# Optimization experiments

Hardware: AMD Instinct MI355X
Metric: run time of the kernel (lower is better)

## Reference

```python
import jax, jax.numpy as jnp
import numpy as np

DIM = 128

def _complex_linear_params(key, dim, scale=0.05):
    k1, k2, k3, k4 = jax.random.split(key, 4)
    Wr = jax.random.normal(k1, (dim, dim), jnp.float32) * scale
    Wi = jax.random.normal(k2, (dim, dim), jnp.float32) * scale
    br = jax.random.normal(k3, (dim,), jnp.float32) * scale
    bi = jax.random.normal(k4, (dim,), jnp.float32) * scale
    return Wr, Wi, br, bi

def setup_inputs() -> dict:
    key = jax.random.key(0)
    ks = jax.random.split(key, 8)
    B, C, Ht, Wt = 8, DIM, 64, 64
    Hs, Ws = 32, 32
    inp = {
        'target_r': jax.random.normal(ks[0], (B, C, Ht, Wt), jnp.float32),
        'target_i': jax.random.normal(ks[1], (B, C, Ht, Wt), jnp.float32),
        'source_r': jax.random.normal(ks[2], (B, C, Hs, Ws), jnp.float32),
        'source_i': jax.random.normal(ks[3], (B, C, Hs, Ws), jnp.float32),
    }
    for name, k in zip(('q', 'k', 'v'), ks[4:7]):
        Wr, Wi, br, bi = _complex_linear_params(k, DIM)
        inp[f'W{name}_r'], inp[f'W{name}_i'] = Wr, Wi
        inp[f'b{name}_r'], inp[f'b{name}_i'] = br, bi
    inp['gamma'] = jnp.float32(0.1)
    return inp

def reference(target_r, target_i, source_r, source_i,
              Wq_r, Wq_i, bq_r, bq_i,
              Wk_r, Wk_i, bk_r, bk_i,
              Wv_r, Wv_i, bv_r, bv_i, gamma):
    B, C, Ht, Wt = target_r.shape
    _, _, Hs, Ws = source_r.shape
    Nt, Ns = Ht * Wt, Hs * Ws
    scale = jnp.float32(C ** 0.5)
    # complex tensors [B, N, C]
    t = (target_r + 1j * target_i).reshape(B, C, Nt).transpose(0, 2, 1)
    s = (source_r + 1j * source_i).reshape(B, C, Ns).transpose(0, 2, 1)
    Wq = Wq_r + 1j * Wq_i; Wk = Wk_r + 1j * Wk_i; Wv = Wv_r + 1j * Wv_i
    Q = jnp.einsum('bnc,dc->bnd', t, Wq) + (bq_r + 1j * bq_i)
    K = jnp.einsum('bmc,dc->bmd', s, Wk) + (bk_r + 1j * bk_i)
    V = jnp.einsum('bmc,dc->bmd', s, Wv) + (bv_r + 1j * bv_i)
    # complex QK^H, keep only real part for softmax
    attn = jnp.einsum('bnd,bmd->bnm', Q, jnp.conj(K))  # [B, Nt, Ns] complex
    w = jax.nn.softmax(attn.real / scale, axis=-1)      # real weights
    out = jnp.einsum('bnm,bmd->bnd', w.astype(V.dtype), V)  # complex [B, Nt, C]
    out = out.transpose(0, 2, 1).reshape(B, C, Ht, Wt)
    return gamma * out
```

## Files before the change

### kernel.cpp

```cpp
#include <hip/hip_runtime.h>
#include <hip/hip_bf16.h>

#define NB 8
#define NC 128
#define NT 4096
#define NS 1024

typedef short bf16x8 __attribute__((ext_vector_type(8)));
typedef float f32x4  __attribute__((ext_vector_type(4)));

#define MFMA16(a, b, c) __builtin_amdgcn_mfma_f32_16x16x32_bf16(a, b, c, 0, 0, 0)

__device__ __forceinline__ short f2b(float x) {
    __hip_bfloat16 h = __float2bfloat16(x);
    return *reinterpret_cast<short*>(&h);
}

__device__ __forceinline__ void gl_lds16(const void* g, void* l) {
    __builtin_amdgcn_global_load_lds(
        (const __attribute__((address_space(1))) unsigned int*)g,
        (__attribute__((address_space(3))) unsigned int*)l, 16, 0, 0);
}

__global__ __launch_bounds__(256) void pack_w_kernel(
    const float* __restrict__ Wqr, const float* __restrict__ Wqi,
    const float* __restrict__ Wkr, const float* __restrict__ Wki,
    const float* __restrict__ Wvr, const float* __restrict__ Wvi,
    __hip_bfloat16* __restrict__ WqT, __hip_bfloat16* __restrict__ WkT,
    __hip_bfloat16* __restrict__ WvT)
{
    const int idx = blockIdx.x * 256 + threadIdx.x;
    const float *Wr, *Wi; __hip_bfloat16* dst; int base;
    if (idx < 65536)       { Wr = Wqr; Wi = Wqi; dst = WqT; base = idx; }
    else if (idx < 131072) { Wr = Wkr; Wi = Wki; dst = WkT; base = idx - 65536; }
    else                   { Wr = Wvr; Wi = Wvi; dst = WvT; base = idx - 131072; }
    const int dp = base >> 8, k = base & 255;
    const int d  = dp & 127;
    float v;
    if (dp < 128) v = (k < 128) ? Wr[d * 128 + k] : -Wi[d * 128 + k - 128];
    else          v = (k < 128) ? Wi[d * 128 + k] :  Wr[d * 128 + k - 128];
    dst[base] = __float2bfloat16(v);
}

__global__ __launch_bounds__(256) void projKV_kernel(
    const float* __restrict__ Xr, const float* __restrict__ Xi,
    const __hip_bfloat16* __restrict__ WkT, const __hip_bfloat16* __restrict__ WvT,
    const float* __restrict__ bkr, const float* __restrict__ bki,
    const float* __restrict__ bvr,
    __hip_bfloat16* __restrict__ Kh, __hip_bfloat16* __restrict__ VrT)
{
    __shared__ __align__(16) char smem[27136];
    const int b   = blockIdx.x & 7;
    const int n0  = (blockIdx.x >> 3) * 32;
    const int tid = threadIdx.x;

    for (int i = tid; i < 32 * 64; i += 256) {
        const int cp = i >> 5, n = i & 31, c = cp * 2;
        const size_t rb = (size_t)(b * NC + c) * NS + n0 + n;
        const unsigned pr = (unsigned short)f2b(Xr[rb]) |
                            ((unsigned)(unsigned short)f2b(Xr[rb + NS]) << 16);
        const unsigned pi = (unsigned short)f2b(Xi[rb]) |
                            ((unsigned)(unsigned short)f2b(Xi[rb + NS]) << 16);
        *(unsigned*)(smem + n * 528 + c * 2)         = pr;
        *(unsigned*)(smem + n * 528 + (128 + c) * 2) = pi;
    }
    __syncthreads();

    const int w = tid >> 6, l15 = tid & 15, q = (tid & 63) >> 4;
    const int r0 = (w & 1) * 16;
    const int g  = w >> 1;

    const char* wp[12];
    #pragma unroll
    for (int jj = 0; jj < 12; ++jj) {
        const int j = g * 12 + jj;
        wp[jj] = (j < 16)
            ? (const char*)WkT + (size_t)(j * 16 + l15) * 512 + q * 16
            : (const char*)WvT + (size_t)((j - 16) * 16 + l15) * 512 + q * 16;
    }

    f32x4 acc[12];
    #pragma unroll
    for (int jj = 0; jj < 12; ++jj) { acc[jj][0]=0.f; acc[jj][1]=0.f; acc[jj][2]=0.f; acc[jj][3]=0.f; }

    #pragma unroll
    for (int t = 0; t < 8; ++t) {
        const bf16x8 af = *(const bf16x8*)(smem + (r0 + l15) * 528 + (t * 32 + q * 8) * 2);
        #pragma unroll
        for (int jj = 0; jj < 12; ++jj) {
            const bf16x8 bf = *(const bf16x8*)(wp[jj] + t * 64);
            acc[jj] = MFMA16(af, bf, acc[jj]);
        }
    }

    #pragma unroll
    for (int jj = 0; jj < 12; ++jj) {
        const int j = g * 12 + jj;
        if (j < 16) {
            const int col = j * 16 + l15;
            const float bv = (col < 128) ? bkr[col] : bki[col - 128];
            #pragma unroll
            for (int r = 0; r < 4; ++r) {
                const int n = n0 + r0 + q * 4 + r;
                Kh[((size_t)(b * NS + n) << 8) + col] = __float2bfloat16(acc[jj][r] + bv);
            }
        } else {
            const int d = (j - 16) * 16 + l15;
            #pragma unroll
            for (int r = 0; r < 4; ++r)
                *(__hip_bfloat16*)(smem + 16896 + d * 80 + (r0 + q * 4 + r) * 2) =
                    __float2bfloat16(acc[jj][r] + bvr[d]);
        }
    }
    __syncthreads();
    for (int i = tid; i < 128 * 4; i += 256) {
        const int d = i >> 2, seg = i & 3;
        const int4 v = *(const int4*)(smem + 16896 + d * 80 + seg * 16);
        *(int4*)((char*)VrT + ((size_t)(b * NC + d) * NS + n0) * 2 + seg * 16) = v;
    }
}

__device__ __forceinline__ void stage_chunk(const char* Kbase, const char* Vbase,
                                            char* buf, int ch, int w, int lane)
{
    const char* ks = Kbase + (size_t)ch * 16384;
    #pragma unroll
    for (int i = 0; i < 4; ++i) {
        const int ml = w * 8 + i * 2 + (lane >> 5);
        const int so = ml * 512 + (((lane & 31) ^ (ml & 7)) << 4);
        gl_lds16(ks + so, buf + (w * 4 + i) * 1024);
    }
    const char* vsrc = Vbase + (size_t)ch * 64;
    #pragma unroll
    for (int i = 0; i < 2; ++i) {
        const int d  = (w + i * 4) * 16 + (lane >> 2);
        const int so = d * 2048 + (((lane & 3) ^ ((lane >> 2) & 3)) << 4);
        gl_lds16(vsrc + so, buf + 16384 + (w + i * 4) * 1024);
    }
}

__global__ __launch_bounds__(256, 2) void attn_mfma_kernel(
    const float* __restrict__ tr_g, const float* __restrict__ ti_g,
    const __hip_bfloat16* __restrict__ WqT,
    const float* __restrict__ bqr, const float* __restrict__ bqi,
    const __hip_bfloat16* __restrict__ Kh, const __hip_bfloat16* __restrict__ VrT,
    const float* __restrict__ gamma_p, float* __restrict__ out)
{
    __shared__ __align__(16) char smem[78848];
    char* As = smem;
    char* ps = smem + 73728;

    const int b    = blockIdx.x & 7;
    const int n0   = (blockIdx.x >> 3) * 64;
    const int tid  = threadIdx.x;
    const int w    = tid >> 6, lane = tid & 63, l15 = tid & 15, q = (tid & 63) >> 4;
    const int row0 = w * 16;
    char* psw = ps + w * 1280;

    for (int i = tid; i < 64 * 64; i += 256) {
        const int cp = i >> 6, n = i & 63, c = cp * 2;
        const size_t rb = (size_t)(b * NC + c) * NT + n0 + n;
        const unsigned pr = (unsigned short)f2b(tr_g[rb]) |
                            ((unsigned)(unsigned short)f2b(tr_g[rb + NT]) << 16);
        const unsigned pi = (unsigned short)f2b(ti_g[rb]) |
                            ((unsigned)(unsigned short)f2b(ti_g[rb + NT]) << 16);
        *(unsigned*)(As + n * 528 + c * 2)         = pr;
        *(unsigned*)(As + n * 528 + (128 + c) * 2) = pi;
    }
    __syncthreads();

    bf16x8 qf[8];
    {
        f32x4 qacc[16];
        #pragma unroll
        for (int j = 0; j < 16; ++j) { qacc[j][0]=0.f; qacc[j][1]=0.f; qacc[j][2]=0.f; qacc[j][3]=0.f; }
        #pragma unroll
        for (int t = 0; t < 8; ++t) {
            const bf16x8 af = *(const bf16x8*)(As + (row0 + l15) * 528 + (t * 32 + q * 8) * 2);
            #pragma unroll
            for (int j = 0; j < 16; ++j) {
                const int col = j * 16 + l15;
                const bf16x8 bf = *(const bf16x8*)((const char*)WqT + col * 512 + (t * 32 + q * 8) * 2);
                qacc[j] = MFMA16(af, bf, qacc[j]);
            }
        }
        const float inv_s = 0.12751744f;
        #pragma unroll
        for (int j = 0; j < 16; ++j) {
            const int col  = j * 16 + l15;
            const float bv = (col < 128) ? bqr[col] : bqi[col - 128];
            #pragma unroll
            for (int r = 0; r < 4; ++r) {
                const int row = row0 + q * 4 + r;
                *(__hip_bfloat16*)(As + row * 528 + col * 2) =
                    __float2bfloat16((qacc[j][r] + bv) * inv_s);
            }
        }
        #pragma unroll
        for (int t = 0; t < 8; ++t)
            qf[t] = *(const bf16x8*)(As + (row0 + l15) * 528 + (t * 32 + q * 8) * 2);
    }
    __syncthreads();

    const char* Kbase = (const char*)Kh + ((size_t)(b * NS) << 9);
    const char* Vbase = (const char*)VrT + (size_t)b * NC * NS * 2;
    char* bA = smem;
    char* bB = smem + 24576;
    char* bC = smem + 49152;

    stage_chunk(Kbase, Vbase, bA, 0, w, lane);
    stage_chunk(Kbase, Vbase, bB, 1, w, lane);

    f32x4 oacc[8];
    #pragma unroll
    for (int j = 0; j < 8; ++j) { oacc[j][0]=0.f; oacc[j][1]=0.f; oacc[j][2]=0.f; oacc[j][3]=0.f; }
    f32x4 lacc;
    lacc[0]=0.f; lacc[1]=0.f; lacc[2]=0.f; lacc[3]=0.f;

    bf16x8 onesf;
    {
        const short ob = (l15 == 0) ? (short)0x3F80 : (short)0;
        #pragma unroll
        for (int e = 0; e < 8; ++e) onesf[e] = ob;
    }

    const int e3   = l15 & 7;
    const int qx   = q ^ (e3 & 3);
    const int eh   = e3 >> 2;
    const int vswz = (q ^ (l15 & 3)) << 4;

    #pragma unroll 1
    for (int ch = 0; ch < 32; ++ch) {
        asm volatile("s_waitcnt vmcnt(6)" ::: "memory");
        __builtin_amdgcn_s_barrier();

        const int sch = (ch + 2 < 32) ? ch + 2 : 31;
        stage_chunk(Kbase, Vbase, bC, sch, w, lane);

        f32x4 s0v, s1v;
        s0v[0]=0.f; s0v[1]=0.f; s0v[2]=0.f; s0v[3]=0.f;
        s1v[0]=0.f; s1v[1]=0.f; s1v[2]=0.f; s1v[3]=0.f;
        #pragma unroll
        for (int t = 0; t < 8; ++t) {
            const int tb = ((t ^ eh) << 6) + (qx << 4);
            const bf16x8 k0 = *(const bf16x8*)(bA + l15 * 512 + tb);
            s0v = MFMA16(qf[t], k0, s0v);
            const bf16x8 k1 = *(const bf16x8*)(bA + (16 + l15) * 512 + tb);
            s1v = MFMA16(qf[t], k1, s1v);
        }

        #pragma unroll
        for (int r = 0; r < 4; ++r) {
            s0v[r] = exp2f(s0v[r]);
            s1v[r] = exp2f(s1v[r]);
        }

        #pragma unroll
        for (int r = 0; r < 4; ++r) {
            *(__hip_bfloat16*)(psw + (q * 4 + r) * 80 + l15 * 2) =
                __float2bfloat16(s0v[r]);
            *(__hip_bfloat16*)(psw + (q * 4 + r) * 80 + (16 + l15) * 2) =
                __float2bfloat16(s1v[r]);
        }

        const bf16x8 pf = *(const bf16x8*)(psw + l15 * 80 + q * 16);
        lacc = MFMA16(pf, onesf, lacc);
        #pragma unroll
        for (int j = 0; j < 8; ++j) {
            const bf16x8 vf = *(const bf16x8*)(bA + 16384 + (j * 16 + l15) * 64 + vswz);
            oacc[j] = MFMA16(pf, vf, oacc[j]);
        }

        char* t0 = bA; bA = bB; bB = bC; bC = t0;
    }

    __syncthreads();
    float* Of = (float*)smem;
    const float g = gamma_p[0];
    #pragma unroll
    for (int r = 0; r < 4; ++r) {
        const float lr = __shfl(lacc[r], q * 16, 64);
        const float inv_l = g / fmaxf(lr, 1e-30f);
        const int m = row0 + q * 4 + r;
        #pragma unroll
        for (int j = 0; j < 8; ++j)
            Of[(j * 16 + l15) * 65 + m] = oacc[j][r] * inv_l;
    }
    __syncthreads();
    float* ob = out + (size_t)b * NC * NT + n0;
    for (int i = tid; i < 128 * 64; i += 256) {
        const int d = i >> 6, m = i & 63;
        ob[(size_t)d * NT + m] = Of[d * 65 + m];
    }
}

extern "C" void kernel_launch(void* const* d_in, const int* in_sizes, int n_in,
                              void* d_out, int out_size, void* d_ws, size_t ws_size,
                              hipStream_t stream)
{
    const float* target_r = (const float*)d_in[0];
    const float* target_i = (const float*)d_in[1];
    const float* source_r = (const float*)d_in[2];
    const float* source_i = (const float*)d_in[3];
    const float* Wq_r = (const float*)d_in[4];
    const float* Wq_i = (const float*)d_in[5];
    const float* bq_r = (const float*)d_in[6];
    const float* bq_i = (const float*)d_in[7];
    const float* Wk_r = (const float*)d_in[8];
    const float* Wk_i = (const float*)d_in[9];
    const float* bk_r = (const float*)d_in[10];
    const float* bk_i = (const float*)d_in[11];
    const float* Wv_r = (const float*)d_in[12];
    const float* Wv_i = (const float*)d_in[13];
    const float* bv_r = (const float*)d_in[14];
    const float* bv_i = (const float*)d_in[15];
    const float* gamma = (const float*)d_in[16];

    char* ws = (char*)d_ws;
    __hip_bfloat16* Kh  = (__hip_bfloat16*)(ws);
    __hip_bfloat16* VrT = (__hip_bfloat16*)(ws + 4194304);
    __hip_bfloat16* WqT = (__hip_bfloat16*)(ws + 6291456);
    __hip_bfloat16* WkT = (__hip_bfloat16*)(ws + 6422528);
    __hip_bfloat16* WvT = (__hip_bfloat16*)(ws + 6553600);

    pack_w_kernel<<<640, 256, 0, stream>>>(Wq_r, Wq_i, Wk_r, Wk_i, Wv_r, Wv_i,
                                           WqT, WkT, WvT);

    projKV_kernel<<<NB * (NS / 32), 256, 0, stream>>>(
        source_r, source_i, WkT, WvT, bk_r, bk_i, bv_r, Kh, VrT);

    attn_mfma_kernel<<<NB * (NT / 64), 256, 0, stream>>>(
        target_r, target_i, WqT, bq_r, bq_i, Kh, VrT, gamma, (float*)d_out);
}
```

Baseline: 198.3 us.

## Double query rows per block to reuse K/V tiles across two row tiles

Each attention block now handles 128 query rows instead of 64, with every wave computing two 16-row tiles that share each K and V fragment read from LDS. The K/V staging moves from a 3-buffer ring with per-chunk barriers to a 4-buffer ring that stages two chunks per iteration, halving the number of barriers. The output store is widened to float4. In exchange, LDS use grows to about 106 KB and launch bounds drop to one block per CU. The grid is also halved to 256 blocks, which lowers occupancy and may leave some CUs idle.

Result: slower. 206.9 us (+4.3%).

```diff
diff --git a/kernel.cpp b/kernel.cpp
--- a/kernel.cpp
+++ b/kernel.cpp
@@ -139,26 +139,26 @@
     }
 }
 
-__global__ __launch_bounds__(256, 2) void attn_mfma_kernel(
+__global__ __launch_bounds__(256, 1) void attn_mfma_kernel(
     const float* __restrict__ tr_g, const float* __restrict__ ti_g,
     const __hip_bfloat16* __restrict__ WqT,
     const float* __restrict__ bqr, const float* __restrict__ bqi,
     const __hip_bfloat16* __restrict__ Kh, const __hip_bfloat16* __restrict__ VrT,
     const float* __restrict__ gamma_p, float* __restrict__ out)
 {
-    __shared__ __align__(16) char smem[78848];
+    __shared__ __align__(16) char smem[108544];
     char* As = smem;
-    char* ps = smem + 73728;
+    char* ps = smem + 98304;
 
     const int b    = blockIdx.x & 7;
-    const int n0   = (blockIdx.x >> 3) * 64;
+    const int n0   = (blockIdx.x >> 3) * 128;
     const int tid  = threadIdx.x;
     const int w    = tid >> 6, lane = tid & 63, l15 = tid & 15, q = (tid & 63) >> 4;
-    const int row0 = w * 16;
-    char* psw = ps + w * 1280;
-
-    for (int i = tid; i < 64 * 64; i += 256) {
-        const int cp = i >> 6, n = i & 63, c = cp * 2;
+    const int row0 = w * 32;
+    char* psw = ps + w * 2560;
+
+    for (int i = tid; i < 128 * 64; i += 256) {
+        const int cp = i >> 7, n = i & 127, c = cp * 2;
         const size_t rb = (size_t)(b * NC + c) * NT + n0 + n;
         const unsigned pr = (unsigned short)f2b(tr_g[rb]) |
                             ((unsigned)(unsigned short)f2b(tr_g[rb + NT]) << 16);
@@ -169,14 +169,17 @@
     }
     __syncthreads();
 
-    bf16x8 qf[8];
-    {
+    bf16x8 qf[2][8];
+    const float inv_s = 0.12751744f;
+    #pragma unroll
+    for (int rt = 0; rt < 2; ++rt) {
+        const int rbase = row0 + rt * 16;
         f32x4 qacc[16];
         #pragma unroll
         for (int j = 0; j < 16; ++j) { qacc[j][0]=0.f; qacc[j][1]=0.f; qacc[j][2]=0.f; qacc[j][3]=0.f; }
         #pragma unroll
         for (int t = 0; t < 8; ++t) {
-            const bf16x8 af = *(const bf16x8*)(As + (row0 + l15) * 528 + (t * 32 + q * 8) * 2);
+            const bf16x8 af = *(const bf16x8*)(As + (rbase + l15) * 528 + (t * 32 + q * 8) * 2);
             #pragma unroll
             for (int j = 0; j < 16; ++j) {
                 const int col = j * 16 + l15;
@@ -184,38 +187,37 @@
                 qacc[j] = MFMA16(af, bf, qacc[j]);
             }
         }
-        const float inv_s = 0.12751744f;
         #pragma unroll
         for (int j = 0; j < 16; ++j) {
             const int col  = j * 16 + l15;
             const float bv = (col < 128) ? bqr[col] : bqi[col - 128];
             #pragma unroll
             for (int r = 0; r < 4; ++r) {
-                const int row = row0 + q * 4 + r;
+                const int row = rbase + q * 4 + r;
                 *(__hip_bfloat16*)(As + row * 528 + col * 2) =
                     __float2bfloat16((qacc[j][r] + bv) * inv_s);
             }
         }
         #pragma unroll
         for (int t = 0; t < 8; ++t)
-            qf[t] = *(const bf16x8*)(As + (row0 + l15) * 528 + (t * 32 + q * 8) * 2);
+            qf[rt][t] = *(const bf16x8*)(As + (rbase + l15) * 528 + (t * 32 + q * 8) * 2);
     }
     __syncthreads();
 
     const char* Kbase = (const char*)Kh + ((size_t)(b * NS) << 9);
     const char* Vbase = (const char*)VrT + (size_t)b * NC * NS * 2;
-    char* bA = smem;
-    char* bB = smem + 24576;
-    char* bC = smem + 49152;
-
-    stage_chunk(Kbase, Vbase, bA, 0, w, lane);
-    stage_chunk(Kbase, Vbase, bB, 1, w, lane);
-
-    f32x4 oacc[8];
-    #pragma unroll
-    for (int j = 0; j < 8; ++j) { oacc[j][0]=0.f; oacc[j][1]=0.f; oacc[j][2]=0.f; oacc[j][3]=0.f; }
-    f32x4 lacc;
-    lacc[0]=0.f; lacc[1]=0.f; lacc[2]=0.f; lacc[3]=0.f;
+
+    stage_chunk(Kbase, Vbase, smem,         0, w, lane);
+    stage_chunk(Kbase, Vbase, smem + 24576, 1, w, lane);
+
+    f32x4 oacc[2][8];
+    #pragma unroll
+    for (int rt = 0; rt < 2; ++rt)
+        #pragma unroll
+        for (int j = 0; j < 8; ++j) { oacc[rt][j][0]=0.f; oacc[rt][j][1]=0.f; oacc[rt][j][2]=0.f; oacc[rt][j][3]=0.f; }
+    f32x4 lacc[2];
+    lacc[0][0]=0.f; lacc[0][1]=0.f; lacc[0][2]=0.f; lacc[0][3]=0.f;
+    lacc[1][0]=0.f; lacc[1][1]=0.f; lacc[1][2]=0.f; lacc[1][3]=0.f;
 
     bf16x8 onesf;
     {
@@ -230,67 +232,83 @@
     const int vswz = (q ^ (l15 & 3)) << 4;
 
     #pragma unroll 1
-    for (int ch = 0; ch < 32; ++ch) {
-        asm volatile("s_waitcnt vmcnt(6)" ::: "memory");
-        __builtin_amdgcn_s_barrier();
-
-        const int sch = (ch + 2 < 32) ? ch + 2 : 31;
-        stage_chunk(Kbase, Vbase, bC, sch, w, lane);
-
-        f32x4 s0v, s1v;
-        s0v[0]=0.f; s0v[1]=0.f; s0v[2]=0.f; s0v[3]=0.f;
-        s1v[0]=0.f; s1v[1]=0.f; s1v[2]=0.f; s1v[3]=0.f;
-        #pragma unroll
-        for (int t = 0; t < 8; ++t) {
-            const int tb = ((t ^ eh) << 6) + (qx << 4);
-            const bf16x8 k0 = *(const bf16x8*)(bA + l15 * 512 + tb);
-            s0v = MFMA16(qf[t], k0, s0v);
-            const bf16x8 k1 = *(const bf16x8*)(bA + (16 + l15) * 512 + tb);
-            s1v = MFMA16(qf[t], k1, s1v);
-        }
-
-        #pragma unroll
-        for (int r = 0; r < 4; ++r) {
-            s0v[r] = exp2f(s0v[r]);
-            s1v[r] = exp2f(s1v[r]);
-        }
-
-        #pragma unroll
-        for (int r = 0; r < 4; ++r) {
-            *(__hip_bfloat16*)(psw + (q * 4 + r) * 80 + l15 * 2) =
-                __float2bfloat16(s0v[r]);
-            *(__hip_bfloat16*)(psw + (q * 4 + r) * 80 + (16 + l15) * 2) =
-                __float2bfloat16(s1v[r]);
-        }
-
-        const bf16x8 pf = *(const bf16x8*)(psw + l15 * 80 + q * 16);
-        lacc = MFMA16(pf, onesf, lacc);
-        #pragma unroll
-        for (int j = 0; j < 8; ++j) {
-            const bf16x8 vf = *(const bf16x8*)(bA + 16384 + (j * 16 + l15) * 64 + vswz);
-            oacc[j] = MFMA16(pf, vf, oacc[j]);
-        }
-
-        char* t0 = bA; bA = bB; bB = bC; bC = t0;
+    for (int it = 0; it < 16; ++it) {
+        const int c0 = it * 2;
+        __syncthreads();
+        if (c0 + 2 < 32) {
+            stage_chunk(Kbase, Vbase, smem + ((c0 + 2) & 3) * 24576, c0 + 2, w, lane);
+            stage_chunk(Kbase, Vbase, smem + ((c0 + 3) & 3) * 24576, c0 + 3, w, lane);
+        }
+
+        #pragma unroll
+        for (int cc = 0; cc < 2; ++cc) {
+            char* bA = smem + ((c0 + cc) & 3) * 24576;
+
+            f32x4 s00, s01, s10, s11;
+            s00[0]=0.f; s00[1]=0.f; s00[2]=0.f; s00[3]=0.f;
+            s01[0]=0.f; s01[1]=0.f; s01[2]=0.f; s01[3]=0.f;
+            s10[0]=0.f; s10[1]=0.f; s10[2]=0.f; s10[3]=0.f;
+            s11[0]=0.f; s11[1]=0.f; s11[2]=0.f; s11[3]=0.f;
+            #pragma unroll
+            for (int t = 0; t < 8; ++t) {
+                const int tb = ((t ^ eh) << 6) + (qx << 4);
+                const bf16x8 k0 = *(const bf16x8*)(bA + l15 * 512 + tb);
+                s00 = MFMA16(qf[0][t], k0, s00);
+                s10 = MFMA16(qf[1][t], k0, s10);
+                const bf16x8 k1 = *(const bf16x8*)(bA + (16 + l15) * 512 + tb);
+                s01 = MFMA16(qf[0][t], k1, s01);
+                s11 = MFMA16(qf[1][t], k1, s11);
+            }
+
+            #pragma unroll
+            for (int r = 0; r < 4; ++r) {
+                *(__hip_bfloat16*)(psw + (q * 4 + r) * 80 + l15 * 2) =
+                    __float2bfloat16(exp2f(s00[r]));
+                *(__hip_bfloat16*)(psw + (q * 4 + r) * 80 + (16 + l15) * 2) =
+                    __float2bfloat16(exp2f(s01[r]));
+                *(__hip_bfloat16*)(psw + 1280 + (q * 4 + r) * 80 + l15 * 2) =
+                    __float2bfloat16(exp2f(s10[r]));
+                *(__hip_bfloat16*)(psw + 1280 + (q * 4 + r) * 80 + (16 + l15) * 2) =
+                    __float2bfloat16(exp2f(s11[r]));
+            }
+
+            bf16x8 vfr[8];
+            #pragma unroll
+            for (int j = 0; j < 8; ++j)
+                vfr[j] = *(const bf16x8*)(bA + 16384 + (j * 16 + l15) * 64 + vswz);
+
+            #pragma unroll
+            for (int rt = 0; rt < 2; ++rt) {
+                const bf16x8 pf = *(const bf16x8*)(psw + rt * 1280 + l15 * 80 + q * 16);
+                lacc[rt] = MFMA16(pf, onesf, lacc[rt]);
+                #pragma unroll
+                for (int j = 0; j < 8; ++j)
+                    oacc[rt][j] = MFMA16(pf, vfr[j], oacc[rt][j]);
+            }
+        }
     }
 
     __syncthreads();
     float* Of = (float*)smem;
     const float g = gamma_p[0];
     #pragma unroll
-    for (int r = 0; r < 4; ++r) {
-        const float lr = __shfl(lacc[r], q * 16, 64);
-        const float inv_l = g / fmaxf(lr, 1e-30f);
-        const int m = row0 + q * 4 + r;
-        #pragma unroll
-        for (int j = 0; j < 8; ++j)
-            Of[(j * 16 + l15) * 65 + m] = oacc[j][r] * inv_l;
+    for (int rt = 0; rt < 2; ++rt) {
+        #pragma unroll
+        for (int r = 0; r < 4; ++r) {
+            const float lr = __shfl(lacc[rt][r], q * 16, 64);
+            const float inv_l = g / fmaxf(lr, 1e-30f);
+            const int m = row0 + rt * 16 + q * 4 + r;
+            #pragma unroll
+            for (int j = 0; j < 8; ++j)
+                Of[(j * 16 + l15) * 132 + m] = oacc[rt][j][r] * inv_l;
+        }
     }
     __syncthreads();
     float* ob = out + (size_t)b * NC * NT + n0;
-    for (int i = tid; i < 128 * 64; i += 256) {
-        const int d = i >> 6, m = i & 63;
-        ob[(size_t)d * NT + m] = Of[d * 65 + m];
+    for (int i = tid; i < 128 * 32; i += 256) {
+        const int d = i >> 5, ms = (i & 31) * 4;
+        const float4 v = *(const float4*)&Of[d * 132 + ms];
+        *(float4*)(ob + (size_t)d * NT + ms) = v;
     }
 }
 
@@ -329,6 +347,6 @@
     projKV_kernel<<<NB * (NS / 32), 256, 0, stream>>>(
         source_r, source_i, WkT, WvT, bk_r, bk_i, bv_r, Kh, VrT);
 
-    attn_mfma_kernel<<<NB * (NT / 64), 256, 0, stream>>>(
+    attn_mfma_kernel<<<NB * (NT / 128), 256, 0, stream>>>(
         target_r, target_i, WqT, bq_r, bq_i, Kh, VrT, gamma, (float*)d_out);
 }
```

## Keep softmax probabilities in registers via transposed QK MFMA and permuted K staging

Applied to the files above, without the earlier changes.

The attention loop swaps the MFMA operand order so the score tile comes out transposed, and permutes which K rows are staged into each LDS slot. Together these let each lane's exp2 outputs be packed straight into the A-operand fragment for the PV and row-sum MFMAs, removing the per-chunk LDS write, wait and read of the probability tile. The K/V projection kernel is also split into 16-row blocks with 6 output tiles per wave, doubling the block count and halving per-thread accumulators. The main risk is a mismatch between the staged K row order and the MFMA output layout, which would silently reorder keys against values.

Result: faster. 190.6 us (-3.9%).

```diff
diff --git a/kernel.cpp b/kernel.cpp
--- a/kernel.cpp
+++ b/kernel.cpp
@@ -49,13 +49,13 @@
     const float* __restrict__ bvr,
     __hip_bfloat16* __restrict__ Kh, __hip_bfloat16* __restrict__ VrT)
 {
-    __shared__ __align__(16) char smem[27136];
+    __shared__ __align__(16) char smem[13568];
     const int b   = blockIdx.x & 7;
-    const int n0  = (blockIdx.x >> 3) * 32;
+    const int n0  = (blockIdx.x >> 3) * 16;
     const int tid = threadIdx.x;
 
-    for (int i = tid; i < 32 * 64; i += 256) {
-        const int cp = i >> 5, n = i & 31, c = cp * 2;
+    for (int i = tid; i < 16 * 64; i += 256) {
+        const int cp = i >> 4, n = i & 15, c = cp * 2;
         const size_t rb = (size_t)(b * NC + c) * NS + n0 + n;
         const unsigned pr = (unsigned short)f2b(Xr[rb]) |
                             ((unsigned)(unsigned short)f2b(Xr[rb + NS]) << 16);
@@ -67,55 +67,53 @@
     __syncthreads();
 
     const int w = tid >> 6, l15 = tid & 15, q = (tid & 63) >> 4;
-    const int r0 = (w & 1) * 16;
-    const int g  = w >> 1;
-
-    const char* wp[12];
-    #pragma unroll
-    for (int jj = 0; jj < 12; ++jj) {
-        const int j = g * 12 + jj;
+
+    const char* wp[6];
+    #pragma unroll
+    for (int jj = 0; jj < 6; ++jj) {
+        const int j = w * 6 + jj;
         wp[jj] = (j < 16)
             ? (const char*)WkT + (size_t)(j * 16 + l15) * 512 + q * 16
             : (const char*)WvT + (size_t)((j - 16) * 16 + l15) * 512 + q * 16;
     }
 
-    f32x4 acc[12];
-    #pragma unroll
-    for (int jj = 0; jj < 12; ++jj) { acc[jj][0]=0.f; acc[jj][1]=0.f; acc[jj][2]=0.f; acc[jj][3]=0.f; }
+    f32x4 acc[6];
+    #pragma unroll
+    for (int jj = 0; jj < 6; ++jj) { acc[jj][0]=0.f; acc[jj][1]=0.f; acc[jj][2]=0.f; acc[jj][3]=0.f; }
 
     #pragma unroll
     for (int t = 0; t < 8; ++t) {
-        const bf16x8 af = *(const bf16x8*)(smem + (r0 + l15) * 528 + (t * 32 + q * 8) * 2);
-        #pragma unroll
-        for (int jj = 0; jj < 12; ++jj) {
+        const bf16x8 af = *(const bf16x8*)(smem + l15 * 528 + (t * 32 + q * 8) * 2);
+        #pragma unroll
+        for (int jj = 0; jj < 6; ++jj) {
             const bf16x8 bf = *(const bf16x8*)(wp[jj] + t * 64);
             acc[jj] = MFMA16(af, bf, acc[jj]);
         }
     }
 
     #pragma unroll
-    for (int jj = 0; jj < 12; ++jj) {
-        const int j = g * 12 + jj;
+    for (int jj = 0; jj < 6; ++jj) {
+        const int j = w * 6 + jj;
         if (j < 16) {
             const int col = j * 16 + l15;
             const float bv = (col < 128) ? bkr[col] : bki[col - 128];
             #pragma unroll
             for (int r = 0; r < 4; ++r) {
-                const int n = n0 + r0 + q * 4 + r;
+                const int n = n0 + q * 4 + r;
                 Kh[((size_t)(b * NS + n) << 8) + col] = __float2bfloat16(acc[jj][r] + bv);
             }
         } else {
             const int d = (j - 16) * 16 + l15;
             #pragma unroll
             for (int r = 0; r < 4; ++r)
-                *(__hip_bfloat16*)(smem + 16896 + d * 80 + (r0 + q * 4 + r) * 2) =
+                *(__hip_bfloat16*)(smem + 8448 + d * 40 + (q * 4 + r) * 2) =
                     __float2bfloat16(acc[jj][r] + bvr[d]);
         }
     }
     __syncthreads();
-    for (int i = tid; i < 128 * 4; i += 256) {
-        const int d = i >> 2, seg = i & 3;
-        const int4 v = *(const int4*)(smem + 16896 + d * 80 + seg * 16);
+    for (int i = tid; i < 128 * 2; i += 256) {
+        const int d = i >> 1, seg = i & 1;
+        const int4 v = *(const int4*)(smem + 8448 + d * 40 + seg * 16);
         *(int4*)((char*)VrT + ((size_t)(b * NC + d) * NS + n0) * 2 + seg * 16) = v;
     }
 }
@@ -127,7 +125,8 @@
     #pragma unroll
     for (int i = 0; i < 4; ++i) {
         const int ml = w * 8 + i * 2 + (lane >> 5);
-        const int so = ml * 512 + (((lane & 31) ^ (ml & 7)) << 4);
+        const int gr = ((ml >> 2) & 3) * 8 + ((ml >> 4) << 2) + (ml & 3);
+        const int so = gr * 512 + (((lane & 31) ^ (ml & 7)) << 4);
         gl_lds16(ks + so, buf + (w * 4 + i) * 1024);
     }
     const char* vsrc = Vbase + (size_t)ch * 64;
@@ -146,16 +145,14 @@
     const __hip_bfloat16* __restrict__ Kh, const __hip_bfloat16* __restrict__ VrT,
     const float* __restrict__ gamma_p, float* __restrict__ out)
 {
-    __shared__ __align__(16) char smem[78848];
+    __shared__ __align__(16) char smem[73728];
     char* As = smem;
-    char* ps = smem + 73728;
 
     const int b    = blockIdx.x & 7;
     const int n0   = (blockIdx.x >> 3) * 64;
     const int tid  = threadIdx.x;
     const int w    = tid >> 6, lane = tid & 63, l15 = tid & 15, q = (tid & 63) >> 4;
     const int row0 = w * 16;
-    char* psw = ps + w * 1280;
 
     for (int i = tid; i < 64 * 64; i += 256) {
         const int cp = i >> 6, n = i & 63, c = cp * 2;
@@ -244,31 +241,23 @@
         for (int t = 0; t < 8; ++t) {
             const int tb = ((t ^ eh) << 6) + (qx << 4);
             const bf16x8 k0 = *(const bf16x8*)(bA + l15 * 512 + tb);
-            s0v = MFMA16(qf[t], k0, s0v);
+            s0v = MFMA16(k0, qf[t], s0v);
             const bf16x8 k1 = *(const bf16x8*)(bA + (16 + l15) * 512 + tb);
-            s1v = MFMA16(qf[t], k1, s1v);
-        }
-
+            s1v = MFMA16(k1, qf[t], s1v);
+        }
+
+        bf16x8 pa;
         #pragma unroll
         for (int r = 0; r < 4; ++r) {
-            s0v[r] = exp2f(s0v[r]);
-            s1v[r] = exp2f(s1v[r]);
-        }
-
-        #pragma unroll
-        for (int r = 0; r < 4; ++r) {
-            *(__hip_bfloat16*)(psw + (q * 4 + r) * 80 + l15 * 2) =
-                __float2bfloat16(s0v[r]);
-            *(__hip_bfloat16*)(psw + (q * 4 + r) * 80 + (16 + l15) * 2) =
-                __float2bfloat16(s1v[r]);
-        }
-
-        const bf16x8 pf = *(const bf16x8*)(psw + l15 * 80 + q * 16);
-        lacc = MFMA16(pf, onesf, lacc);
+            pa[r]     = f2b(exp2f(s0v[r]));
+            pa[4 + r] = f2b(exp2f(s1v[r]));
+        }
+
+        lacc = MFMA16(pa, onesf, lacc);
         #pragma unroll
         for (int j = 0; j < 8; ++j) {
             const bf16x8 vf = *(const bf16x8*)(bA + 16384 + (j * 16 + l15) * 64 + vswz);
-            oacc[j] = MFMA16(pf, vf, oacc[j]);
+            oacc[j] = MFMA16(pa, vf, oacc[j]);
         }
 
         char* t0 = bA; bA = bB; bB = bC; bC = t0;
@@ -326,7 +315,7 @@
     pack_w_kernel<<<640, 256, 0, stream>>>(Wq_r, Wq_i, Wk_r, Wk_i, Wv_r, Wv_i,
                                            WqT, WkT, WvT);
 
-    projKV_kernel<<<NB * (NS / 32), 256, 0, stream>>>(
+    projKV_kernel<<<NB * (NS / 16), 256, 0, stream>>>(
         source_r, source_i, WkT, WvT, bk_r, bk_i, bv_r, Kh, VrT);
 
     attn_mfma_kernel<<<NB * (NT / 64), 256, 0, stream>>>(
```
